# Kernel tuning notes

Measured on AMD Instinct MI355X. Metric: run time of the kernel, lower is better.

The kernel has to match this reference:

```python
import jax, jax.numpy as jnp
import numpy as np

EMB = 512
HEADS = 8
HEAD_DIM = EMB // HEADS


def setup_inputs() -> dict:
    key = jax.random.key(0)
    ks = jax.random.split(key, 9)
    s = 1.0 / np.sqrt(EMB)
    return {
        "x": jax.random.normal(ks[0], (4, 2048, EMB), dtype=jnp.float32),
        "Wq": jax.random.uniform(ks[1], (EMB, EMB), jnp.float32, -s, s),
        "bq": jax.random.uniform(ks[2], (EMB,), jnp.float32, -s, s),
        "Wk": jax.random.uniform(ks[3], (EMB, EMB), jnp.float32, -s, s),
        "bk": jax.random.uniform(ks[4], (EMB,), jnp.float32, -s, s),
        "Wv": jax.random.uniform(ks[5], (EMB, EMB), jnp.float32, -s, s),
        "bv": jax.random.uniform(ks[6], (EMB,), jnp.float32, -s, s),
        "Wp": jax.random.uniform(ks[7], (EMB, EMB), jnp.float32, -s, s),
        "bp": jax.random.uniform(ks[8], (EMB,), jnp.float32, -s, s),
    }


def _split_heads(t):
    b, n, _ = t.shape
    return t.reshape(b, n, HEADS, HEAD_DIM).transpose(0, 2, 1, 3)  # b h n d


def reference(x, Wq, bq, Wk, bk, Wv, bv, Wp, bp):
    q = _split_heads(x @ Wq.T + bq)
    k = _split_heads(x @ Wk.T + bk)
    v = _split_heads(x @ Wv.T + bv)
    energy = jnp.einsum("bhqd,bhkd->bhqk", q, k)
    # NOTE: original applies softmax to UNSCALED logits, then divides probs by sqrt(emb)
    att = jax.nn.softmax(energy, axis=-1) / jnp.sqrt(jnp.float32(EMB))
    out = jnp.einsum("bhqk,bhkd->bhqd", att, v)
    b, h, n, d = out.shape
    out = out.transpose(0, 2, 1, 3).reshape(b, n, h * d)
    return out @ Wp.T + bp
```

## Files before the change

kernel.cpp:

```cpp
#include <hip/hip_runtime.h>
#include <math.h>
#include <stdint.h>

#define SEQ  2048
#define LOG2E 1.4426950408889634f

typedef __attribute__((ext_vector_type(4))) float f32x4;
typedef __attribute__((ext_vector_type(16))) float f32x16;
typedef __attribute__((ext_vector_type(8))) short bf16x8;

template <int V> struct IC { static constexpr int value = V; };

__device__ __forceinline__ unsigned packbf(float a, float b) {
    return __builtin_amdgcn_perm(__float_as_uint(b) + 0x8000u,
                                 __float_as_uint(a) + 0x8000u, 0x07060302u);
}

__global__ __launch_bounds__(256) void cvt_kernel(
    const float* __restrict__ x,  const float* __restrict__ wq,
    const float* __restrict__ wk, const float* __restrict__ wv,
    const float* __restrict__ wp,
    unsigned short* __restrict__ xb,  unsigned short* __restrict__ wqb,
    unsigned short* __restrict__ wkb, unsigned short* __restrict__ wvb,
    unsigned short* __restrict__ wpb)
{
    const int c = blockIdx.x * 256 + threadIdx.x;
    const float* s;
    unsigned short* d;
    int off;
    if (c < 524288) {
        s = x; d = xb; off = c;
    } else {
        const int cc = c - 524288;
        const int wsel = cc >> 15;
        off = cc & 32767;
        s = wsel == 0 ? wq : wsel == 1 ? wk : wsel == 2 ? wv : wp;
        d = wsel == 0 ? wqb : wsel == 1 ? wkb : wsel == 2 ? wvb : wpb;
    }
    const float4* sp = (const float4*)s + (size_t)off * 2;
    const float4 a = sp[0], b = sp[1];
    uint4 p;
    p.x = packbf(a.x, a.y); p.y = packbf(a.z, a.w);
    p.z = packbf(b.x, b.y); p.w = packbf(b.z, b.w);
    *((uint4*)d + off) = p;
}

__global__ __launch_bounds__(256, 3) void qkv_kernel(
    const unsigned short* __restrict__ xb, const unsigned short* __restrict__ wqb,
    const unsigned short* __restrict__ wkb, const unsigned short* __restrict__ wvb,
    const float* __restrict__ bq, const float* __restrict__ bk,
    const float* __restrict__ bv,
    unsigned short* __restrict__ Qw, unsigned short* __restrict__ Kw,
    unsigned short* __restrict__ VTw)
{
    __shared__ __align__(16) unsigned short smem[8192];
    unsigned short* As = smem;
    unsigned short* Bs = smem + 4096;

    const int t = threadIdx.x;
    const int w = t >> 6, lane = t & 63, quad = (t >> 4) & 3, l15 = t & 15;
    const int wr = w >> 1, wc = w & 1;
    const int m0 = blockIdx.y * 128;
    const int n0 = blockIdx.x * 128;
    const int which = n0 >> 9;
    const unsigned short* wbase = which == 0 ? wqb : (which == 1 ? wkb : wvb);
    const int nrow = n0 & 511;

    const int ar = t >> 2, akq = t & 3;
    const unsigned short* ax = xb + (size_t)(m0 + ar) * 512 + akq * 8;
    const unsigned short* bx = wbase + (size_t)(nrow + ar) * 512 + akq * 8;
    const int lws = (ar & 15) | (akq << 4);
    const int off0 = (ar >> 4) * 512 + lws * 8;
    const int off1 = off0 + 4 * 512;

    f32x4 acc[4][4];
#pragma unroll
    for (int mt = 0; mt < 4; ++mt)
#pragma unroll
        for (int nt = 0; nt < 4; ++nt) acc[mt][nt] = (f32x4){0.f, 0.f, 0.f, 0.f};

    uint4 ra0, ra1, rb0, rb1;
    auto loadt = [&](int k0) {
        ra0 = *(const uint4*)(ax + k0);
        ra1 = *(const uint4*)(ax + 32768 + k0);
        rb0 = *(const uint4*)(bx + k0);
        rb1 = *(const uint4*)(bx + 32768 + k0);
    };
    auto writet = [&]() {
        *(uint4*)(As + off0) = ra0;
        *(uint4*)(As + off1) = ra1;
        *(uint4*)(Bs + off0) = rb0;
        *(uint4*)(Bs + off1) = rb1;
    };

    loadt(0);
    auto kloop = [&](auto TRC) {
        constexpr int TR = decltype(TRC)::value;
        for (int ki = 0; ki < 16; ++ki) {
            writet();
            if (ki < 15) loadt((ki + 1) * 32);
            __syncthreads();
            bf16x8 af[4], bfr[4];
#pragma unroll
            for (int mt = 0; mt < 4; ++mt)
                af[mt] = *(const bf16x8*)(As + ((wr * 4 + mt) * 64 + lane) * 8);
#pragma unroll
            for (int nt = 0; nt < 4; ++nt)
                bfr[nt] = *(const bf16x8*)(Bs + ((wc * 4 + nt) * 64 + lane) * 8);
#pragma unroll
            for (int mt = 0; mt < 4; ++mt)
#pragma unroll
                for (int nt = 0; nt < 4; ++nt) {
                    if (TR)
                        acc[mt][nt] = __builtin_amdgcn_mfma_f32_16x16x32_bf16(
                            bfr[nt], af[mt], acc[mt][nt], 0, 0, 0);
                    else
                        acc[mt][nt] = __builtin_amdgcn_mfma_f32_16x16x32_bf16(
                            af[mt], bfr[nt], acc[mt][nt], 0, 0, 0);
                }
            if (ki < 15) __syncthreads();
        }
    };
    if (which < 2) kloop(IC<1>{});
    else           kloop(IC<0>{});

    if (which == 2) {
#pragma unroll
        for (int nt = 0; nt < 4; ++nt) {
            const int n = n0 + wc * 64 + nt * 16 + l15;
            const float bias = bv[n & 511];
            const int h = (n >> 6) & 7, d = n & 63;
#pragma unroll
            for (int mt = 0; mt < 4; ++mt) {
                const int mb = m0 + wr * 64 + mt * 16 + quad * 4;
                const int bi = mb >> 11, ns = mb & 2047;
                const int bhl = bi * 8 + h;
                const f32x4 v = acc[mt][nt];
                uint2 pk;
                pk.x = packbf(v[0] + bias, v[1] + bias);
                pk.y = packbf(v[2] + bias, v[3] + bias);
                const size_t off =
                    ((size_t)(bhl * 32 + (ns >> 6)) * 8 + ((d >> 5) << 2) +
                     ((ns >> 4) & 3)) * 512 +
                    ((d & 31) << 3) + ((ns & 8) << 5) + (ns & 7);
                *(uint2*)(VTw + off) = pk;
            }
        }
    } else {
        const float sc = which ? 1.f : LOG2E;
        const float* bpt = which ? bk : bq;
        unsigned short* base = which ? Kw : Qw;
#pragma unroll
        for (int nt = 0; nt < 4; ++nt) {
            const int nb = n0 + wc * 64 + nt * 16 + quad * 4;
            const f32x4 bvv = *(const f32x4*)(bpt + (nb & 511));
            const int h = (nb >> 6) & 7, d0 = nb & 63;
#pragma unroll
            for (int mt = 0; mt < 4; ++mt) {
                const int nsg = m0 + wr * 64 + mt * 16 + l15;
                const int bi = nsg >> 11, ns = nsg & 2047;
                const int bhl = bi * 8 + h;
                const f32x4 v = acc[mt][nt];
                uint2 pk;
                pk.x = packbf((v[0] + bvv[0]) * sc, (v[1] + bvv[1]) * sc);
                pk.y = packbf((v[2] + bvv[2]) * sc, (v[3] + bvv[3]) * sc);
                const size_t off =
                    ((size_t)(bhl * 64 + (ns >> 5)) * 4 + (d0 >> 4)) * 512 +
                    ((d0 & 8) << 5) + ((ns & 31) << 3) + (d0 & 7);
                *(uint2*)(base + off) = pk;
            }
        }
    }
}

__global__ __launch_bounds__(256, 3) void outproj_kernel(
    const unsigned short* __restrict__ Aw, const unsigned short* __restrict__ wpb,
    const float* __restrict__ bp, float* __restrict__ out)
{
    __shared__ __align__(16) unsigned short smem[6144];
    unsigned short* As = smem;
    unsigned short* Bs = smem + 4096;

    const int t = threadIdx.x;
    const int w = t >> 6, lane = t & 63, quad = (t >> 4) & 3, l15 = t & 15;
    const int wr = w >> 1, wc = w & 1;
    const int m0 = blockIdx.y * 128;
    const int n0 = blockIdx.x * 64;

    const int ar = t >> 2, akq = t & 3;
    const unsigned short* ap = Aw + (size_t)(m0 + ar) * 512 + akq * 8;
    const unsigned short* bx = wpb + (size_t)(n0 + ar) * 512 + akq * 8;
    const int lws = (ar & 15) | (akq << 4);
    const int off0 = (ar >> 4) * 512 + lws * 8;
    const int off1 = off0 + 4 * 512;
    const int boff = (ar >> 4) * 512 + lws * 8;

    f32x4 acc[4][2];
#pragma unroll
    for (int mt = 0; mt < 4; ++mt)
#pragma unroll
        for (int nt = 0; nt < 2; ++nt) acc[mt][nt] = (f32x4){0.f, 0.f, 0.f, 0.f};

    uint4 ra0, ra1, rb0;
    auto loadt = [&](int k0) {
        ra0 = *(const uint4*)(ap + k0);
        ra1 = *(const uint4*)(ap + 32768 + k0);
        rb0 = *(const uint4*)(bx + k0);
    };
    auto writet = [&]() {
        *(uint4*)(As + off0) = ra0;
        *(uint4*)(As + off1) = ra1;
        *(uint4*)(Bs + boff) = rb0;
    };

    loadt(0);
    for (int ki = 0; ki < 16; ++ki) {
        writet();
        if (ki < 15) loadt((ki + 1) * 32);
        __syncthreads();
        bf16x8 af[4], bfr[2];
#pragma unroll
        for (int mt = 0; mt < 4; ++mt)
            af[mt] = *(const bf16x8*)(As + ((wr * 4 + mt) * 64 + lane) * 8);
#pragma unroll
        for (int nt = 0; nt < 2; ++nt)
            bfr[nt] = *(const bf16x8*)(Bs + ((wc * 2 + nt) * 64 + lane) * 8);
#pragma unroll
        for (int mt = 0; mt < 4; ++mt)
#pragma unroll
            for (int nt = 0; nt < 2; ++nt)
                acc[mt][nt] = __builtin_amdgcn_mfma_f32_16x16x32_bf16(
                    af[mt], bfr[nt], acc[mt][nt], 0, 0, 0);
        if (ki < 15) __syncthreads();
    }

#pragma unroll
    for (int nt = 0; nt < 2; ++nt) {
        const int n = n0 + wc * 32 + nt * 16 + l15;
        const float bias = bp[n];
#pragma unroll
        for (int mt = 0; mt < 4; ++mt) {
            const int mb = m0 + wr * 64 + mt * 16 + quad * 4;
            const f32x4 v = acc[mt][nt];
#pragma unroll
            for (int r = 0; r < 4; ++r)
                out[(size_t)(mb + r) * 512 + n] = v[r] + bias;
        }
    }
}

#define ATTN_STEP(STC, STN, JT)                                                \
    do {                                                                       \
        const int jt_ = (JT);                                                  \
        bf16x8 vc[4];                                                          \
        _Pragma("unroll")                                                      \
        for (int dg = 0; dg < 2; ++dg)                                         \
            _Pragma("unroll")                                                  \
            for (int p = 0; p < 2; ++p)                                        \
                vc[dg * 2 + p] = *(const bf16x8*)(                             \
                    Vp + (size_t)jt_ * 4096 + (dg * 4 + jh * 2 + p) * 512);    \
        STN = zero;                                                            \
        __builtin_amdgcn_s_setprio(1);                                         \
        _Pragma("unroll")                                                      \
        for (int kt = 0; kt < 4; ++kt)                                         \
            STN = __builtin_amdgcn_mfma_f32_32x32x16_bf16(kc[kt], qf[kt],      \
                                                          STN, 0, 0, 0);       \
        __builtin_amdgcn_s_setprio(0);                                         \
        const int jn_ = (jt_ < 30) ? jt_ + 2 : 31;                             \
        _Pragma("unroll")                                                      \
        for (int c = 0; c < 4; ++c)                                            \
            kc[c] = *(const bf16x8*)(Kp + (size_t)jn_ * 4096 + c * 512);       \
        _Pragma("unroll")                                                      \
        for (int r = 0; r < 16; ++r)                                           \
            STC[r] = __builtin_amdgcn_exp2f(STC[r]);                           \
        {                                                                      \
            float s01 = STC[0] + STC[1],   s23 = STC[2] + STC[3];              \
            float s45 = STC[4] + STC[5],   s67 = STC[6] + STC[7];              \
            float s89 = STC[8] + STC[9],   sAB = STC[10] + STC[11];            \
            float sCD = STC[12] + STC[13], sEF = STC[14] + STC[15];            \
            lpart += ((s01 + s23) + (s45 + s67)) + ((s89 + sAB) + (sCD + sEF));\
        }                                                                      \
        _Pragma("unroll")                                                      \
        for (int p = 0; p < 2; ++p) {                                          \
            const int r0 = p * 8;                                              \
            unsigned a0, a1, b0, b1;                                           \
            asm("v_cvt_pk_bf16_f32 %0, %1, %2"                                 \
                : "=v"(a0) : "v"(STC[r0 + 0]), "v"(STC[r0 + 1]));              \
            asm("v_cvt_pk_bf16_f32 %0, %1, %2"                                 \
                : "=v"(a1) : "v"(STC[r0 + 2]), "v"(STC[r0 + 3]));              \
            asm("v_cvt_pk_bf16_f32 %0, %1, %2"                                 \
                : "=v"(b0) : "v"(STC[r0 + 4]), "v"(STC[r0 + 5]));              \
            asm("v_cvt_pk_bf16_f32 %0, %1, %2"                                 \
                : "=v"(b1) : "v"(STC[r0 + 6]), "v"(STC[r0 + 7]));              \
            asm("v_permlane32_swap_b32 %0, %1" : "+v"(a0), "+v"(b0));          \
            asm("v_permlane32_swap_b32 %0, %1" : "+v"(a1), "+v"(b1));          \
            union { unsigned u[4]; bf16x8 v; } pb;                             \
            pb.u[0] = a0;                                                      \
            pb.u[1] = a1;                                                      \
            pb.u[2] = b0;                                                      \
            pb.u[3] = b1;                                                      \
            __builtin_amdgcn_s_setprio(1);                                     \
            Ot[0] = __builtin_amdgcn_mfma_f32_32x32x16_bf16(vc[0 + p], pb.v,   \
                                                            Ot[0], 0, 0, 0);   \
            Ot[1] = __builtin_amdgcn_mfma_f32_32x32x16_bf16(vc[2 + p], pb.v,   \
                                                            Ot[1], 0, 0, 0);   \
            __builtin_amdgcn_s_setprio(0);                                     \
        }                                                                      \
    } while (0)

__global__ __launch_bounds__(512, 2) void attn_kernel(
    const unsigned short* __restrict__ Qf, const unsigned short* __restrict__ Kf,
    const unsigned short* __restrict__ Vf, unsigned short* __restrict__ Ow)
{
    __shared__ float cb[8448];
    const int t = threadIdx.x;
    const int w = t >> 6, lane = t & 63;
    const int l31 = lane & 31, hlf = lane >> 5;
    const int qi = w >> 1, jh = w & 1;

    const int bh = blockIdx.x;
    const int qblk = blockIdx.y;
    const int q0 = qblk * 128;

    const unsigned short* Kp = Kf + (size_t)bh * 131072 + (jh * 4) * 512 + lane * 8;
    const unsigned short* Vp = Vf + (size_t)bh * 131072 + lane * 8;

    const int qgg = qblk * 4 + qi;
    const unsigned short* Qp = Qf + ((size_t)(bh * 64 + qgg) * 4) * 512 + lane * 8;
    bf16x8 qf[4];
#pragma unroll
    for (int kt = 0; kt < 4; ++kt)
        qf[kt] = *(const bf16x8*)(Qp + kt * 512);

    f32x16 zero;
#pragma unroll
    for (int r = 0; r < 16; ++r) zero[r] = 0.f;

    float lpart = 0.f;
    f32x16 Ot[2];
    Ot[0] = zero; Ot[1] = zero;

    bf16x8 kc[4];
#pragma unroll
    for (int c = 0; c < 4; ++c)
        kc[c] = *(const bf16x8*)(Kp + c * 512);

    f32x16 stA = zero, stB = zero;
#pragma unroll
    for (int kt = 0; kt < 4; ++kt)
        stA = __builtin_amdgcn_mfma_f32_32x32x16_bf16(kc[kt], qf[kt], stA, 0, 0, 0);
#pragma unroll
    for (int c = 0; c < 4; ++c)
        kc[c] = *(const bf16x8*)(Kp + 4096 + c * 512);

    for (int jt = 0; jt < 32; jt += 2) {
        ATTN_STEP(stA, stB, jt);
        ATTN_STEP(stB, stA, jt + 1);
    }

    if (jh == 1) {
#pragma unroll
        for (int dg = 0; dg < 2; ++dg) {
            const int cidx = (qi * 2 + dg) * 4;
#pragma unroll
            for (int k = 0; k < 4; ++k) {
                float4 v = make_float4(
                    Ot[dg][k * 4 + 0], Ot[dg][k * 4 + 1],
                    Ot[dg][k * 4 + 2], Ot[dg][k * 4 + 3]);
                *(float4*)(cb + (cidx + k) * 256 + lane * 4) = v;
            }
        }
        cb[8192 + qi * 64 + lane] = lpart;
    }
    __syncthreads();
    if (jh == 0) {
        const int bi = bh >> 3, h = bh & 7;
#pragma unroll
        for (int dg = 0; dg < 2; ++dg) {
            const int cidx = (qi * 2 + dg) * 4;
#pragma unroll
            for (int k = 0; k < 4; ++k) {
                const float4 v = *(const float4*)(cb + (cidx + k) * 256 + lane * 4);
                Ot[dg][k * 4 + 0] += v.x;
                Ot[dg][k * 4 + 1] += v.y;
                Ot[dg][k * 4 + 2] += v.z;
                Ot[dg][k * 4 + 3] += v.w;
            }
        }
        float lv = lpart + cb[8192 + qi * 64 + lane];
        lv += __shfl_xor(lv, 32);
        const float inv = 1.0f / (lv * 22.627416997969522f);

        const int ns = q0 + qi * 32 + l31;
        unsigned short* dst = Ow + ((size_t)bi * SEQ + ns) * 512 + h * 64 + hlf * 4;
#pragma unroll
        for (int dg = 0; dg < 2; ++dg)
#pragma unroll
            for (int rb2 = 0; rb2 < 4; ++rb2) {
                uint2 pk;
                pk.x = packbf(Ot[dg][rb2 * 4 + 0] * inv,
                              Ot[dg][rb2 * 4 + 1] * inv);
                pk.y = packbf(Ot[dg][rb2 * 4 + 2] * inv,
                              Ot[dg][rb2 * 4 + 3] * inv);
                *(uint2*)(dst + dg * 32 + rb2 * 8) = pk;
            }
    }
}

extern "C" void kernel_launch(void* const* d_in, const int* in_sizes, int n_in,
                              void* d_out, int out_size, void* d_ws, size_t ws_size,
                              hipStream_t stream)
{
    const float* x  = (const float*)d_in[0];
    const float* Wq = (const float*)d_in[1];
    const float* bq = (const float*)d_in[2];
    const float* Wk = (const float*)d_in[3];
    const float* bk = (const float*)d_in[4];
    const float* Wv = (const float*)d_in[5];
    const float* bv = (const float*)d_in[6];
    const float* Wp = (const float*)d_in[7];
    const float* bp = (const float*)d_in[8];

    unsigned short* ws = (unsigned short*)d_ws;
    unsigned short* Qw  = ws;
    unsigned short* Kw  = Qw + 4194304;
    unsigned short* VTw = Kw + 4194304;
    unsigned short* Owb = VTw + 4194304;
    unsigned short* xb  = Owb;
    unsigned short* wqb = Owb + 4194304;
    unsigned short* wkb = wqb + 262144;
    unsigned short* wvb = wkb + 262144;
    unsigned short* wpb = wvb + 262144;

    cvt_kernel<<<dim3(2560), 256, 0, stream>>>(
        x, Wq, Wk, Wv, Wp, xb, wqb, wkb, wvb, wpb);
    qkv_kernel<<<dim3(12, 64), 256, 0, stream>>>(
        xb, wqb, wkb, wvb, bq, bk, bv, Qw, Kw, VTw);
    attn_kernel<<<dim3(32, 16), 512, 0, stream>>>(Qw, Kw, VTw, Owb);
    outproj_kernel<<<dim3(8, 64), 256, 0, stream>>>(Owb, wpb, bp, (float*)d_out);
}
```

Before: 162.9 us.

## Use direct global-to-LDS loads with double buffering in GEMMs; prefetch V tiles in attention

```diff
diff --git a/kernel.cpp b/kernel.cpp
--- a/kernel.cpp
+++ b/kernel.cpp
@@ -14,6 +14,12 @@
 __device__ __forceinline__ unsigned packbf(float a, float b) {
     return __builtin_amdgcn_perm(__float_as_uint(b) + 0x8000u,
                                  __float_as_uint(a) + 0x8000u, 0x07060302u);
+}
+
+__device__ __forceinline__ void gload16(const unsigned short* g, unsigned short* l) {
+    __builtin_amdgcn_global_load_lds(
+        (const __attribute__((address_space(1))) unsigned int*)g,
+        (__attribute__((address_space(3))) unsigned int*)l, 16, 0, 0);
 }
 
 __global__ __launch_bounds__(256) void cvt_kernel(
@@ -53,9 +59,7 @@
     unsigned short* __restrict__ Qw, unsigned short* __restrict__ Kw,
     unsigned short* __restrict__ VTw)
 {
-    __shared__ __align__(16) unsigned short smem[8192];
-    unsigned short* As = smem;
-    unsigned short* Bs = smem + 4096;
+    __shared__ __align__(16) unsigned short smem[16384];
 
     const int t = threadIdx.x;
     const int w = t >> 6, lane = t & 63, quad = (t >> 4) & 3, l15 = t & 15;
@@ -66,12 +70,8 @@
     const unsigned short* wbase = which == 0 ? wqb : (which == 1 ? wkb : wvb);
     const int nrow = n0 & 511;
 
-    const int ar = t >> 2, akq = t & 3;
-    const unsigned short* ax = xb + (size_t)(m0 + ar) * 512 + akq * 8;
-    const unsigned short* bx = wbase + (size_t)(nrow + ar) * 512 + akq * 8;
-    const int lws = (ar & 15) | (akq << 4);
-    const int off0 = (ar >> 4) * 512 + lws * 8;
-    const int off1 = off0 + 4 * 512;
+    const unsigned short* axg = xb + (size_t)(m0 + w * 16 + (lane & 15)) * 512 + ((lane >> 4) * 8);
+    const unsigned short* bxg = wbase + (size_t)(nrow + w * 16 + (lane & 15)) * 512 + ((lane >> 4) * 8);
 
     f32x4 acc[4][4];
 #pragma unroll
@@ -79,27 +79,24 @@
 #pragma unroll
         for (int nt = 0; nt < 4; ++nt) acc[mt][nt] = (f32x4){0.f, 0.f, 0.f, 0.f};
 
-    uint4 ra0, ra1, rb0, rb1;
-    auto loadt = [&](int k0) {
-        ra0 = *(const uint4*)(ax + k0);
-        ra1 = *(const uint4*)(ax + 32768 + k0);
-        rb0 = *(const uint4*)(bx + k0);
-        rb1 = *(const uint4*)(bx + 32768 + k0);
+    auto stage = [&](int b, int k0) {
+        unsigned short* Ad = smem + b * 8192 + w * 512;
+        unsigned short* Bd = Ad + 4096;
+        gload16(axg + k0, Ad);
+        gload16(axg + 32768 + k0, Ad + 2048);
+        gload16(bxg + k0, Bd);
+        gload16(bxg + 32768 + k0, Bd + 2048);
     };
-    auto writet = [&]() {
-        *(uint4*)(As + off0) = ra0;
-        *(uint4*)(As + off1) = ra1;
-        *(uint4*)(Bs + off0) = rb0;
-        *(uint4*)(Bs + off1) = rb1;
-    };
-
-    loadt(0);
+
+    stage(0, 0);
+    int cur = 0;
     auto kloop = [&](auto TRC) {
         constexpr int TR = decltype(TRC)::value;
         for (int ki = 0; ki < 16; ++ki) {
-            writet();
-            if (ki < 15) loadt((ki + 1) * 32);
             __syncthreads();
+            if (ki < 15) stage(cur ^ 1, (ki + 1) * 32);
+            const unsigned short* As = smem + cur * 8192;
+            const unsigned short* Bs = As + 4096;
             bf16x8 af[4], bfr[4];
 #pragma unroll
             for (int mt = 0; mt < 4; ++mt)
@@ -118,7 +115,7 @@
                         acc[mt][nt] = __builtin_amdgcn_mfma_f32_16x16x32_bf16(
                             af[mt], bfr[nt], acc[mt][nt], 0, 0, 0);
                 }
-            if (ki < 15) __syncthreads();
+            cur ^= 1;
         }
     };
     if (which < 2) kloop(IC<1>{});
@@ -177,9 +174,7 @@
     const unsigned short* __restrict__ Aw, const unsigned short* __restrict__ wpb,
     const float* __restrict__ bp, float* __restrict__ out)
 {
-    __shared__ __align__(16) unsigned short smem[6144];
-    unsigned short* As = smem;
-    unsigned short* Bs = smem + 4096;
+    __shared__ __align__(16) unsigned short smem[12288];
 
     const int t = threadIdx.x;
     const int w = t >> 6, lane = t & 63, quad = (t >> 4) & 3, l15 = t & 15;
@@ -187,13 +182,8 @@
     const int m0 = blockIdx.y * 128;
     const int n0 = blockIdx.x * 64;
 
-    const int ar = t >> 2, akq = t & 3;
-    const unsigned short* ap = Aw + (size_t)(m0 + ar) * 512 + akq * 8;
-    const unsigned short* bx = wpb + (size_t)(n0 + ar) * 512 + akq * 8;
-    const int lws = (ar & 15) | (akq << 4);
-    const int off0 = (ar >> 4) * 512 + lws * 8;
-    const int off1 = off0 + 4 * 512;
-    const int boff = (ar >> 4) * 512 + lws * 8;
+    const unsigned short* apg = Aw + (size_t)(m0 + w * 16 + (lane & 15)) * 512 + ((lane >> 4) * 8);
+    const unsigned short* bpg = wpb + (size_t)(n0 + w * 16 + (lane & 15)) * 512 + ((lane >> 4) * 8);
 
     f32x4 acc[4][2];
 #pragma unroll
@@ -201,23 +191,21 @@
 #pragma unroll
         for (int nt = 0; nt < 2; ++nt) acc[mt][nt] = (f32x4){0.f, 0.f, 0.f, 0.f};
 
-    uint4 ra0, ra1, rb0;
-    auto loadt = [&](int k0) {
-        ra0 = *(const uint4*)(ap + k0);
-        ra1 = *(const uint4*)(ap + 32768 + k0);
-        rb0 = *(const uint4*)(bx + k0);
+    auto stage = [&](int b, int k0) {
+        unsigned short* Ad = smem + b * 6144 + w * 512;
+        unsigned short* Bd = smem + b * 6144 + 4096 + w * 512;
+        gload16(apg + k0, Ad);
+        gload16(apg + 32768 + k0, Ad + 2048);
+        gload16(bpg + k0, Bd);
     };
-    auto writet = [&]() {
-        *(uint4*)(As + off0) = ra0;
-        *(uint4*)(As + off1) = ra1;
-        *(uint4*)(Bs + boff) = rb0;
-    };
-
-    loadt(0);
+
+    stage(0, 0);
+    int cur = 0;
     for (int ki = 0; ki < 16; ++ki) {
-        writet();
-        if (ki < 15) loadt((ki + 1) * 32);
         __syncthreads();
+        if (ki < 15) stage(cur ^ 1, (ki + 1) * 32);
+        const unsigned short* As = smem + cur * 6144;
+        const unsigned short* Bs = As + 4096;
         bf16x8 af[4], bfr[2];
 #pragma unroll
         for (int mt = 0; mt < 4; ++mt)
@@ -231,7 +219,7 @@
             for (int nt = 0; nt < 2; ++nt)
                 acc[mt][nt] = __builtin_amdgcn_mfma_f32_16x16x32_bf16(
                     af[mt], bfr[nt], acc[mt][nt], 0, 0, 0);
-        if (ki < 15) __syncthreads();
+        cur ^= 1;
     }
 
 #pragma unroll
@@ -249,16 +237,16 @@
     }
 }
 
-#define ATTN_STEP(STC, STN, JT)                                                \
+#define ATTN_STEP(STC, STN, VCC, VCN, JT)                                      \
     do {                                                                       \
         const int jt_ = (JT);                                                  \
-        bf16x8 vc[4];                                                          \
+        const int jv_ = (jt_ < 31) ? jt_ + 1 : 31;                             \
         _Pragma("unroll")                                                      \
         for (int dg = 0; dg < 2; ++dg)                                         \
             _Pragma("unroll")                                                  \
             for (int p = 0; p < 2; ++p)                                        \
-                vc[dg * 2 + p] = *(const bf16x8*)(                             \
-                    Vp + (size_t)jt_ * 4096 + (dg * 4 + jh * 2 + p) * 512);    \
+                VCN[dg * 2 + p] = *(const bf16x8*)(                            \
+                    Vp + (size_t)jv_ * 4096 + (dg * 4 + jh * 2 + p) * 512);    \
         STN = zero;                                                            \
         __builtin_amdgcn_s_setprio(1);                                         \
         _Pragma("unroll")                                                      \
@@ -300,9 +288,9 @@
             pb.u[2] = b0;                                                      \
             pb.u[3] = b1;                                                      \
             __builtin_amdgcn_s_setprio(1);                                     \
-            Ot[0] = __builtin_amdgcn_mfma_f32_32x32x16_bf16(vc[0 + p], pb.v,   \
+            Ot[0] = __builtin_amdgcn_mfma_f32_32x32x16_bf16(VCC[0 + p], pb.v,  \
                                                             Ot[0], 0, 0, 0);   \
-            Ot[1] = __builtin_amdgcn_mfma_f32_32x32x16_bf16(vc[2 + p], pb.v,   \
+            Ot[1] = __builtin_amdgcn_mfma_f32_32x32x16_bf16(VCC[2 + p], pb.v,  \
                                                             Ot[1], 0, 0, 0);   \
             __builtin_amdgcn_s_setprio(0);                                     \
         }                                                                      \
@@ -345,6 +333,13 @@
     for (int c = 0; c < 4; ++c)
         kc[c] = *(const bf16x8*)(Kp + c * 512);
 
+    bf16x8 vcA[4], vcB[4];
+#pragma unroll
+    for (int dg = 0; dg < 2; ++dg)
+#pragma unroll
+        for (int p = 0; p < 2; ++p)
+            vcA[dg * 2 + p] = *(const bf16x8*)(Vp + (dg * 4 + jh * 2 + p) * 512);
+
     f32x16 stA = zero, stB = zero;
 #pragma unroll
     for (int kt = 0; kt < 4; ++kt)
@@ -354,8 +349,8 @@
         kc[c] = *(const bf16x8*)(Kp + 4096 + c * 512);
 
     for (int jt = 0; jt < 32; jt += 2) {
-        ATTN_STEP(stA, stB, jt);
-        ATTN_STEP(stB, stA, jt + 1);
+        ATTN_STEP(stA, stB, vcA, vcB, jt);
+        ATTN_STEP(stB, stA, vcB, vcA, jt + 1);
     }
 
     if (jh == 1) {
```

After: 171.9 us. 5.5% more time.
